# Kernel optimization log

Measured on AMD Instinct MI355X. Metric: run time of the kernel, lower is better.

Reference implementation:

```python
import jax, jax.numpy as jnp
import numpy as np

EPS = 1e-5
SCALE = 1.0 / np.float32(np.sqrt(64.0))  # 1/sqrt(d_Q)


def layernorm(x):
    # fresh nn.LayerNorm each call: gamma=1, beta=0
    m = jnp.mean(x, axis=-1, keepdims=True)
    v = jnp.mean((x - m) ** 2, axis=-1, keepdims=True)
    return (x - m) * jax.lax.rsqrt(v + EPS)


def setup_inputs() -> dict:
    key = jax.random.key(0)
    ks = jax.random.split(key, 8)
    B, S, D, H, F = 32, 512, 256, 64, 256
    w = 0.05
    return {
        "x": jax.random.normal(ks[0], (B, S, D), jnp.float32),
        "mask": jax.random.randint(ks[1], (B, 6, S, S), 0, 2).astype(jnp.int32),
        "Wq": jax.random.normal(ks[2], (6, D, H), jnp.float32) * w,
        "Wk": jax.random.normal(ks[3], (6, D, H), jnp.float32) * w,
        "Wv": jax.random.normal(ks[4], (6, D, H), jnp.float32) * w,
        "Wfc": jax.random.normal(ks[5], (6, H, D), jnp.float32) * w,
        "W1": jax.random.normal(ks[6], (D, F), jnp.float32) * w,
        "W2": jax.random.normal(ks[7], (F, D), jnp.float32) * w,
    }


def reference(x, mask, Wq, Wk, Wv, Wfc, W1, W2):
    m = mask.astype(bool)                                   # [B,6,S,S]
    # batched over the 6 relation branches (r axis)
    Q = jnp.einsum('bsd,rdh->brsh', x, Wq)                  # [B,6,S,64]
    K = jnp.einsum('bsd,rdh->brsh', x, Wk)
    V = jnp.einsum('bsd,rdh->brsh', x, Wv)
    score = jnp.einsum('brsh,brth->brst', Q, K) * SCALE     # [B,6,S,S]
    score = jnp.where(m, jnp.float32(-1e9), score)
    attn = jax.nn.softmax(score, axis=-1)
    attn = jnp.where(m, jnp.float32(0.0), attn)             # post-softmax zeroing
    ctx = jnp.einsum('brst,brth->brsh', attn, V)            # [B,6,S,64]
    proj = jnp.einsum('brsh,rhd->brsd', ctx, Wfc)           # [B,6,S,256]
    branch = layernorm(proj + x[:, None, :, :])             # residual + fresh LN per branch
    s = jnp.sum(branch, axis=1)                             # sum of 6 branches [B,S,256]
    ffn = jnp.maximum(jnp.einsum('bsd,df->bsf', s, W1), 0.0)
    ffn = jnp.einsum('bsf,fd->bsd', ffn, W2)
    return layernorm(ffn + s)
```

## Files before the change

kernel.cpp:

```cpp
#include <hip/hip_runtime.h>
#include <hip/hip_bf16.h>

#define BB 32
#define RR 6
#define SS 512
#define DD 256
#define HH 64
#define FF 256

typedef short  short8 __attribute__((ext_vector_type(8)));
typedef short  short4v __attribute__((ext_vector_type(4)));
typedef float  f32x4  __attribute__((ext_vector_type(4)));
typedef unsigned short ushort_t;
typedef unsigned int   uint_t;

__device__ __forceinline__ ushort_t f2bf(float f) {
    __hip_bfloat16 b = __float2bfloat16(f);
    return __builtin_bit_cast(ushort_t, b);
}
__device__ __forceinline__ float bf2f(ushort_t u) {
    return __bfloat162float(__builtin_bit_cast(__hip_bfloat16, u));
}

__global__ __launch_bounds__(256) void convert_all_kernel(
        const float* __restrict__ x,
        const float* __restrict__ Wq, const float* __restrict__ Wk, const float* __restrict__ Wv,
        const float* __restrict__ Wfc, const float* __restrict__ W1, const float* __restrict__ W2,
        ushort_t* __restrict__ xb, ushort_t* __restrict__ wT, ushort_t* __restrict__ w1T,
        ushort_t* __restrict__ w2T, ushort_t* __restrict__ wfcT) {
    int bid = blockIdx.x;
    if (bid < 4096) {
        int gid = bid * 256 + threadIdx.x;
        float4 fv = ((const float4*)x)[gid];
        short4v o;
        o[0] = (short)f2bf(fv.x); o[1] = (short)f2bf(fv.y);
        o[2] = (short)f2bf(fv.z); o[3] = (short)f2bf(fv.w);
        *(short4v*)(xb + (size_t)gid * 4) = o;
        return;
    }
    int gid = (bid - 4096) * 256 + threadIdx.x;
    if (gid < 294912) {
        int n = gid >> 8, d = gid & 255;
        int r = n / 192, rem = n % 192;
        int which = rem >> 6, h = rem & 63;
        const float* W = which == 0 ? Wq : which == 1 ? Wk : Wv;
        wT[gid] = f2bf(W[(size_t)r * DD * HH + (size_t)d * HH + h]);
    } else if (gid < 360448) {
        int gg = gid - 294912;
        int f = gg >> 8, d = gg & 255;
        w1T[gg] = f2bf(W1[(size_t)d * FF + f]);
    } else if (gid < 425984) {
        int gg = gid - 360448;
        int d = gg >> 8, f = gg & 255;
        w2T[gg] = f2bf(W2[(size_t)f * DD + d]);
    } else {
        int gg = gid - 425984;
        int n = gg >> 6, h = gg & 63;
        int r = n >> 8, d = n & 255;
        wfcT[gg] = f2bf(Wfc[((size_t)r * HH + h) * DD + d]);
    }
}

__global__ __launch_bounds__(256) void qkv_mfma_kernel(
        const ushort_t* __restrict__ xb, const ushort_t* __restrict__ wT,
        ushort_t* __restrict__ q, ushort_t* __restrict__ k, ushort_t* __restrict__ v) {
    int bid = blockIdx.x;
    int id = (bid & 7) * 288 + (bid >> 3);
    int rt = id / 18, cw = id % 18;
    int r = cw / 3, which = cw % 3;

    int tid = threadIdx.x;
    int wv = tid >> 6, l = tid & 63;
    int wr = wv >> 1, wc = wv & 1;
    int g = l >> 4, lc = l & 15;

    const ushort_t* Arow = xb + ((size_t)(rt * 128 + wr * 64 + lc)) * DD + g * 8;
    const ushort_t* Brow = wT + ((size_t)(cw * 64 + wc * 32 + lc)) * DD + g * 8;

    f32x4 acc[4][2] = {};
    #pragma unroll 4
    for (int ks = 0; ks < 8; ++ks) {
        short8 af[4], bf[2];
        #pragma unroll
        for (int m = 0; m < 4; ++m)
            af[m] = *(const short8*)(Arow + (size_t)m * 16 * DD + ks * 32);
        #pragma unroll
        for (int n = 0; n < 2; ++n)
            bf[n] = *(const short8*)(Brow + (size_t)n * 16 * DD + ks * 32);
        #pragma unroll
        for (int m = 0; m < 4; ++m)
            #pragma unroll
            for (int n = 0; n < 2; ++n)
                acc[m][n] = __builtin_amdgcn_mfma_f32_16x16x32_bf16(af[m], bf[n], acc[m][n], 0, 0, 0);
    }

    ushort_t* outb = which == 0 ? q : which == 1 ? k : v;
    #pragma unroll
    for (int m = 0; m < 4; ++m) {
        #pragma unroll
        for (int reg = 0; reg < 4; ++reg) {
            int grow = rt * 128 + wr * 64 + m * 16 + g * 4 + reg;
            int orow = ((grow >> 9) * RR + r) * SS + (grow & (SS - 1));
            #pragma unroll
            for (int n = 0; n < 2; ++n)
                outb[(size_t)orow * HH + wc * 32 + n * 16 + lc] = f2bf(acc[m][n][reg]);
        }
    }
}

__global__ __launch_bounds__(256) void attn_mfma_kernel(
        const ushort_t* __restrict__ q, const ushort_t* __restrict__ k,
        const ushort_t* __restrict__ v, const int* __restrict__ mask,
        ushort_t* __restrict__ ctx) {
    int wg = blockIdx.x;
    int id = (wg & 7) * 192 + (wg >> 3);
    int br = id >> 3, qt = id & 7;

    __shared__ ushort_t K_lds[64 * 72];
    __shared__ ushort_t VT_lds[64 * 66];
    __shared__ ushort_t P_lds[4][16 * 72];

    int tid = threadIdx.x;
    int wv = tid >> 6, l = tid & 63;
    int g = l >> 4, lc = l & 15;

    int q0 = qt * 64 + wv * 16;
    const size_t base_kv = (size_t)br * SS * HH;

    short8 qf[2];
    #pragma unroll
    for (int kk = 0; kk < 2; ++kk)
        qf[kk] = *(const short8*)(q + ((size_t)br * SS + q0 + lc) * HH + kk * 32 + g * 8);

    f32x4 O[4] = {{0,0,0,0},{0,0,0,0},{0,0,0,0},{0,0,0,0}};
    float lrun[4] = {0.f, 0.f, 0.f, 0.f};

    const int* mb = mask + ((size_t)br * SS + q0) * SS;

    for (int t0 = 0; t0 < SS; t0 += 64) {
        __syncthreads();
        for (int c = tid; c < 512; c += 256) {
            int t = c >> 3, c8 = (c & 7) * 8;
            *(short8*)&K_lds[t * 72 + c8] =
                *(const short8*)(k + base_kv + (size_t)(t0 + t) * HH + c8);
        }
        {
            int h = tid & 63, tseg = tid >> 6;
            #pragma unroll
            for (int jj = 0; jj < 8; ++jj) {
                int t = tseg * 16 + jj * 2;
                uint_t p0 = v[base_kv + (size_t)(t0 + t) * HH + h];
                uint_t p1 = v[base_kv + (size_t)(t0 + t + 1) * HH + h];
                *(uint_t*)&VT_lds[h * 66 + t] = p0 | (p1 << 16);
            }
        }
        __syncthreads();

        f32x4 S[4];
        #pragma unroll
        for (int tc = 0; tc < 4; ++tc) {
            f32x4 c = {0, 0, 0, 0};
            #pragma unroll
            for (int kk = 0; kk < 2; ++kk) {
                short8 bf = *(const short8*)&K_lds[(tc * 16 + lc) * 72 + kk * 32 + g * 8];
                c = __builtin_amdgcn_mfma_f32_16x16x32_bf16(qf[kk], bf, c, 0, 0, 0);
            }
            S[tc] = c;
        }

        float psum[4] = {0.f, 0.f, 0.f, 0.f};
        ushort_t* Pw = P_lds[wv];
        #pragma unroll
        for (int tc = 0; tc < 4; ++tc)
            #pragma unroll
            for (int reg = 0; reg < 4; ++reg) {
                int qrow = 4 * g + reg;
                int mv = mb[(size_t)qrow * SS + t0 + tc * 16 + lc];
                float p = mv ? 0.f : __expf(S[tc][reg] * 0.125f);
                psum[reg] += p;
                Pw[(4 * g + reg) * 72 + tc * 16 + lc] = f2bf(p);
            }
        #pragma unroll
        for (int reg = 0; reg < 4; ++reg) {
            float ps = psum[reg];
            ps += __shfl_xor(ps, 1, 64);
            ps += __shfl_xor(ps, 2, 64);
            ps += __shfl_xor(ps, 4, 64);
            ps += __shfl_xor(ps, 8, 64);
            lrun[reg] += ps;
        }
        asm volatile("s_waitcnt lgkmcnt(0)" ::: "memory");

        #pragma unroll
        for (int ts = 0; ts < 2; ++ts) {
            short8 pa = *(const short8*)&Pw[lc * 72 + ts * 32 + g * 8];
            #pragma unroll
            for (int hb = 0; hb < 4; ++hb) {
                short8 vbf = *(const short8*)&VT_lds[(hb * 16 + lc) * 66 + ts * 32 + g * 8];
                O[hb] = __builtin_amdgcn_mfma_f32_16x16x32_bf16(pa, vbf, O[hb], 0, 0, 0);
            }
        }
    }

    ushort_t* cb = ctx + ((size_t)br * SS + q0) * HH;
    #pragma unroll
    for (int reg = 0; reg < 4; ++reg) {
        float inv = lrun[reg] > 0.f ? 1.f / lrun[reg] : 0.f;
        #pragma unroll
        for (int hb = 0; hb < 4; ++hb)
            cb[(size_t)(4 * g + reg) * HH + hb * 16 + lc] = f2bf(O[hb][reg] * inv);
    }
}

__global__ __launch_bounds__(256) void fused_tail_kernel(
        const ushort_t* __restrict__ ctx, const ushort_t* __restrict__ wfcT,
        const float* __restrict__ x, const ushort_t* __restrict__ w1T,
        const ushort_t* __restrict__ w2T, float* __restrict__ out) {
    int bid = blockIdx.x;
    int rt = (bid & 7) * 128 + (bid >> 3);
    int row0 = rt * 16;
    int b = row0 >> 9, s0 = row0 & (SS - 1);

    int tid = threadIdx.x;
    int wc = tid >> 6, l = tid & 63;
    int g = l >> 4, lc = l & 15;
    int col0 = wc * 64;

    __shared__ ushort_t s_lds[16 * 264];
    __shared__ ushort_t h_lds[16 * 264];
    __shared__ float red_s[16][4];
    __shared__ float red_q[16][4];

    float xres[4][4];
    #pragma unroll
    for (int hb = 0; hb < 4; ++hb)
        #pragma unroll
        for (int reg = 0; reg < 4; ++reg)
            xres[hb][reg] = x[((size_t)row0 + g * 4 + reg) * DD + col0 + hb * 16 + lc];

    float acc_ln[4][4] = {};

    for (int r = 0; r < RR; ++r) {
        const ushort_t* Abase = ctx + (((size_t)b * RR + r) * SS + s0 + lc) * HH + g * 8;
        const ushort_t* Bbase = wfcT + ((size_t)r * 256 + col0 + lc) * HH + g * 8;
        f32x4 acc[4] = {};
        #pragma unroll
        for (int ks = 0; ks < 2; ++ks) {
            short8 af = *(const short8*)(Abase + ks * 32);
            #pragma unroll
            for (int hb = 0; hb < 4; ++hb) {
                short8 bf = *(const short8*)(Bbase + (size_t)hb * 16 * HH + ks * 32);
                acc[hb] = __builtin_amdgcn_mfma_f32_16x16x32_bf16(af, bf, acc[hb], 0, 0, 0);
            }
        }

        float psum[4] = {0, 0, 0, 0}, psq[4] = {0, 0, 0, 0};
        #pragma unroll
        for (int hb = 0; hb < 4; ++hb)
            #pragma unroll
            for (int reg = 0; reg < 4; ++reg) {
                float vv = acc[hb][reg] + xres[hb][reg];
                acc[hb][reg] = vv;
                psum[reg] += vv;
                psq[reg]  += vv * vv;
            }
        #pragma unroll
        for (int reg = 0; reg < 4; ++reg) {
            #pragma unroll
            for (int off = 1; off <= 8; off <<= 1) {
                psum[reg] += __shfl_xor(psum[reg], off, 64);
                psq[reg]  += __shfl_xor(psq[reg],  off, 64);
            }
        }
        if (lc == 0) {
            #pragma unroll
            for (int reg = 0; reg < 4; ++reg) {
                red_s[g * 4 + reg][wc] = psum[reg];
                red_q[g * 4 + reg][wc] = psq[reg];
            }
        }
        __syncthreads();
        #pragma unroll
        for (int reg = 0; reg < 4; ++reg) {
            int row = g * 4 + reg;
            float sum = red_s[row][0] + red_s[row][1] + red_s[row][2] + red_s[row][3];
            float sq  = red_q[row][0] + red_q[row][1] + red_q[row][2] + red_q[row][3];
            float mean = sum * (1.f / 256.f);
            float var  = sq * (1.f / 256.f) - mean * mean;
            float inv  = rsqrtf(var + 1e-5f);
            #pragma unroll
            for (int hb = 0; hb < 4; ++hb)
                acc_ln[hb][reg] += (acc[hb][reg] - mean) * inv;
        }
        __syncthreads();
    }

    #pragma unroll
    for (int hb = 0; hb < 4; ++hb)
        #pragma unroll
        for (int reg = 0; reg < 4; ++reg)
            s_lds[(g * 4 + reg) * 264 + col0 + hb * 16 + lc] = f2bf(acc_ln[hb][reg]);
    __syncthreads();

    f32x4 acc1[4] = {};
    #pragma unroll
    for (int ks = 0; ks < 8; ++ks) {
        short8 af = *(const short8*)&s_lds[lc * 264 + ks * 32 + g * 8];
        #pragma unroll
        for (int hb = 0; hb < 4; ++hb) {
            short8 bf = *(const short8*)(w1T + (size_t)(col0 + hb * 16 + lc) * DD + ks * 32 + g * 8);
            acc1[hb] = __builtin_amdgcn_mfma_f32_16x16x32_bf16(af, bf, acc1[hb], 0, 0, 0);
        }
    }
    #pragma unroll
    for (int hb = 0; hb < 4; ++hb)
        #pragma unroll
        for (int reg = 0; reg < 4; ++reg)
            h_lds[(g * 4 + reg) * 264 + col0 + hb * 16 + lc] = f2bf(fmaxf(acc1[hb][reg], 0.f));
    __syncthreads();

    f32x4 acc2[4] = {};
    #pragma unroll
    for (int ks = 0; ks < 8; ++ks) {
        short8 af = *(const short8*)&h_lds[lc * 264 + ks * 32 + g * 8];
        #pragma unroll
        for (int hb = 0; hb < 4; ++hb) {
            short8 bf = *(const short8*)(w2T + (size_t)(col0 + hb * 16 + lc) * FF + ks * 32 + g * 8);
            acc2[hb] = __builtin_amdgcn_mfma_f32_16x16x32_bf16(af, bf, acc2[hb], 0, 0, 0);
        }
    }

    float psum[4] = {0, 0, 0, 0}, psq[4] = {0, 0, 0, 0};
    #pragma unroll
    for (int hb = 0; hb < 4; ++hb)
        #pragma unroll
        for (int reg = 0; reg < 4; ++reg) {
            float vv = acc2[hb][reg] + bf2f(s_lds[(g * 4 + reg) * 264 + col0 + hb * 16 + lc]);
            acc2[hb][reg] = vv;
            psum[reg] += vv;
            psq[reg]  += vv * vv;
        }
    #pragma unroll
    for (int reg = 0; reg < 4; ++reg) {
        #pragma unroll
        for (int off = 1; off <= 8; off <<= 1) {
            psum[reg] += __shfl_xor(psum[reg], off, 64);
            psq[reg]  += __shfl_xor(psq[reg],  off, 64);
        }
    }
    if (lc == 0) {
        #pragma unroll
        for (int reg = 0; reg < 4; ++reg) {
            red_s[g * 4 + reg][wc] = psum[reg];
            red_q[g * 4 + reg][wc] = psq[reg];
        }
    }
    __syncthreads();
    #pragma unroll
    for (int reg = 0; reg < 4; ++reg) {
        int row = g * 4 + reg;
        float sum = red_s[row][0] + red_s[row][1] + red_s[row][2] + red_s[row][3];
        float sq  = red_q[row][0] + red_q[row][1] + red_q[row][2] + red_q[row][3];
        float mean = sum * (1.f / 256.f);
        float var  = sq * (1.f / 256.f) - mean * mean;
        float inv  = rsqrtf(var + 1e-5f);
        #pragma unroll
        for (int hb = 0; hb < 4; ++hb)
            out[((size_t)row0 + row) * DD + col0 + hb * 16 + lc] = (acc2[hb][reg] - mean) * inv;
    }
}

extern "C" void kernel_launch(void* const* d_in, const int* in_sizes, int n_in,
                              void* d_out, int out_size, void* d_ws, size_t ws_size,
                              hipStream_t stream) {
    const float* x    = (const float*)d_in[0];
    const int*   mask = (const int*)  d_in[1];
    const float* Wq   = (const float*)d_in[2];
    const float* Wk   = (const float*)d_in[3];
    const float* Wv   = (const float*)d_in[4];
    const float* Wfc  = (const float*)d_in[5];
    const float* W1   = (const float*)d_in[6];
    const float* W2   = (const float*)d_in[7];
    float* out = (float*)d_out;

    const size_t QKV = (size_t)BB * RR * SS * HH;
    const size_t BSD = (size_t)BB * SS * DD;
    ushort_t* qb  = (ushort_t*)d_ws;
    ushort_t* kb  = qb + QKV;
    ushort_t* vb  = kb + QKV;
    ushort_t* ctx = vb + QKV;
    ushort_t* xb  = ctx + QKV;
    ushort_t* wT  = xb + BSD;
    ushort_t* w1T = wT + (size_t)1152 * 256;
    ushort_t* w2T = w1T + 65536;
    ushort_t* wfcT = w2T + 65536;

    convert_all_kernel<<<6144, 256, 0, stream>>>(x, Wq, Wk, Wv, Wfc, W1, W2,
                                                 xb, wT, w1T, w2T, wfcT);
    qkv_mfma_kernel  <<<2304, 256, 0, stream>>>(xb, wT, qb, kb, vb);
    attn_mfma_kernel <<<BB * RR * 8, 256, 0, stream>>>(qb, kb, vb, mask, ctx);
    fused_tail_kernel<<<1024, 256, 0, stream>>>(ctx, wfcT, x, w1T, w2T, out);
}
```

Measured before the change: 191.9 us.

## Give each wave full rows in tail kernel to drop cross-wave LayerNorm reductions

```diff
diff --git a/kernel.cpp b/kernel.cpp
--- a/kernel.cpp
+++ b/kernel.cpp
@@ -212,55 +212,54 @@
     }
 }
 
-__global__ __launch_bounds__(256) void fused_tail_kernel(
+__global__ __launch_bounds__(128) void fused_tail_kernel(
         const ushort_t* __restrict__ ctx, const ushort_t* __restrict__ wfcT,
         const float* __restrict__ x, const ushort_t* __restrict__ w1T,
         const ushort_t* __restrict__ w2T, float* __restrict__ out) {
     int bid = blockIdx.x;
-    int rt = (bid & 7) * 128 + (bid >> 3);
-    int row0 = rt * 16;
+    int sw = (bid & 7) * 64 + (bid >> 3);
+    int tid = threadIdx.x;
+    int wv = tid >> 6, l = tid & 63;
+    int g = l >> 4, lc = l & 15;
+
+    int row0 = (sw * 2 + wv) * 16;
     int b = row0 >> 9, s0 = row0 & (SS - 1);
 
-    int tid = threadIdx.x;
-    int wc = tid >> 6, l = tid & 63;
-    int g = l >> 4, lc = l & 15;
-    int col0 = wc * 64;
-
-    __shared__ ushort_t s_lds[16 * 264];
-    __shared__ ushort_t h_lds[16 * 264];
-    __shared__ float red_s[16][4];
-    __shared__ float red_q[16][4];
-
-    float xres[4][4];
-    #pragma unroll
-    for (int hb = 0; hb < 4; ++hb)
+    __shared__ ushort_t s_lds[2][16 * 264];
+    __shared__ ushort_t h_lds[2][16 * 264];
+    ushort_t* S = s_lds[wv];
+    ushort_t* Hh = h_lds[wv];
+
+    float xres[16][4];
+    #pragma unroll
+    for (int n = 0; n < 16; ++n)
         #pragma unroll
         for (int reg = 0; reg < 4; ++reg)
-            xres[hb][reg] = x[((size_t)row0 + g * 4 + reg) * DD + col0 + hb * 16 + lc];
-
-    float acc_ln[4][4] = {};
+            xres[n][reg] = x[((size_t)row0 + g * 4 + reg) * DD + n * 16 + lc];
+
+    float acc_ln[16][4] = {};
 
     for (int r = 0; r < RR; ++r) {
         const ushort_t* Abase = ctx + (((size_t)b * RR + r) * SS + s0 + lc) * HH + g * 8;
-        const ushort_t* Bbase = wfcT + ((size_t)r * 256 + col0 + lc) * HH + g * 8;
-        f32x4 acc[4] = {};
+        const ushort_t* Bbase = wfcT + ((size_t)r * 256 + lc) * HH + g * 8;
+        f32x4 acc[16] = {};
         #pragma unroll
         for (int ks = 0; ks < 2; ++ks) {
             short8 af = *(const short8*)(Abase + ks * 32);
             #pragma unroll
-            for (int hb = 0; hb < 4; ++hb) {
-                short8 bf = *(const short8*)(Bbase + (size_t)hb * 16 * HH + ks * 32);
-                acc[hb] = __builtin_amdgcn_mfma_f32_16x16x32_bf16(af, bf, acc[hb], 0, 0, 0);
+            for (int n = 0; n < 16; ++n) {
+                short8 bf = *(const short8*)(Bbase + (size_t)n * 16 * HH + ks * 32);
+                acc[n] = __builtin_amdgcn_mfma_f32_16x16x32_bf16(af, bf, acc[n], 0, 0, 0);
             }
         }
 
         float psum[4] = {0, 0, 0, 0}, psq[4] = {0, 0, 0, 0};
         #pragma unroll
-        for (int hb = 0; hb < 4; ++hb)
+        for (int n = 0; n < 16; ++n)
             #pragma unroll
             for (int reg = 0; reg < 4; ++reg) {
-                float vv = acc[hb][reg] + xres[hb][reg];
-                acc[hb][reg] = vv;
+                float vv = acc[n][reg] + xres[n][reg];
+                acc[n][reg] = vv;
                 psum[reg] += vv;
                 psq[reg]  += vv * vv;
             }
@@ -271,72 +270,57 @@
                 psum[reg] += __shfl_xor(psum[reg], off, 64);
                 psq[reg]  += __shfl_xor(psq[reg],  off, 64);
             }
-        }
-        if (lc == 0) {
-            #pragma unroll
-            for (int reg = 0; reg < 4; ++reg) {
-                red_s[g * 4 + reg][wc] = psum[reg];
-                red_q[g * 4 + reg][wc] = psq[reg];
-            }
-        }
-        __syncthreads();
+            float mean = psum[reg] * (1.f / 256.f);
+            float var  = psq[reg] * (1.f / 256.f) - mean * mean;
+            float inv  = rsqrtf(var + 1e-5f);
+            #pragma unroll
+            for (int n = 0; n < 16; ++n)
+                acc_ln[n][reg] += (acc[n][reg] - mean) * inv;
+        }
+    }
+
+    #pragma unroll
+    for (int n = 0; n < 16; ++n)
+        #pragma unroll
+        for (int reg = 0; reg < 4; ++reg)
+            S[(g * 4 + reg) * 264 + n * 16 + lc] = f2bf(acc_ln[n][reg]);
+    __syncthreads();
+
+    f32x4 acc1[16] = {};
+    #pragma unroll
+    for (int ks = 0; ks < 8; ++ks) {
+        short8 af = *(const short8*)&S[lc * 264 + ks * 32 + g * 8];
+        #pragma unroll
+        for (int n = 0; n < 16; ++n) {
+            short8 bf = *(const short8*)(w1T + (size_t)(n * 16 + lc) * DD + ks * 32 + g * 8);
+            acc1[n] = __builtin_amdgcn_mfma_f32_16x16x32_bf16(af, bf, acc1[n], 0, 0, 0);
+        }
+    }
+    #pragma unroll
+    for (int n = 0; n < 16; ++n)
+        #pragma unroll
+        for (int reg = 0; reg < 4; ++reg)
+            Hh[(g * 4 + reg) * 264 + n * 16 + lc] = f2bf(fmaxf(acc1[n][reg], 0.f));
+    __syncthreads();
+
+    f32x4 acc2[16] = {};
+    #pragma unroll
+    for (int ks = 0; ks < 8; ++ks) {
+        short8 af = *(const short8*)&Hh[lc * 264 + ks * 32 + g * 8];
+        #pragma unroll
+        for (int n = 0; n < 16; ++n) {
+            short8 bf = *(const short8*)(w2T + (size_t)(n * 16 + lc) * FF + ks * 32 + g * 8);
+            acc2[n] = __builtin_amdgcn_mfma_f32_16x16x32_bf16(af, bf, acc2[n], 0, 0, 0);
+        }
+    }
+
+    float psum[4] = {0, 0, 0, 0}, psq[4] = {0, 0, 0, 0};
+    #pragma unroll
+    for (int n = 0; n < 16; ++n)
         #pragma unroll
         for (int reg = 0; reg < 4; ++reg) {
-            int row = g * 4 + reg;
-            float sum = red_s[row][0] + red_s[row][1] + red_s[row][2] + red_s[row][3];
-            float sq  = red_q[row][0] + red_q[row][1] + red_q[row][2] + red_q[row][3];
-            float mean = sum * (1.f / 256.f);
-            float var  = sq * (1.f / 256.f) - mean * mean;
-            float inv  = rsqrtf(var + 1e-5f);
-            #pragma unroll
-            for (int hb = 0; hb < 4; ++hb)
-                acc_ln[hb][reg] += (acc[hb][reg] - mean) * inv;
-        }
-        __syncthreads();
-    }
-
-    #pragma unroll
-    for (int hb = 0; hb < 4; ++hb)
-        #pragma unroll
-        for (int reg = 0; reg < 4; ++reg)
-            s_lds[(g * 4 + reg) * 264 + col0 + hb * 16 + lc] = f2bf(acc_ln[hb][reg]);
-    __syncthreads();
-
-    f32x4 acc1[4] = {};
-    #pragma unroll
-    for (int ks = 0; ks < 8; ++ks) {
-        short8 af = *(const short8*)&s_lds[lc * 264 + ks * 32 + g * 8];
-        #pragma unroll
-        for (int hb = 0; hb < 4; ++hb) {
-            short8 bf = *(const short8*)(w1T + (size_t)(col0 + hb * 16 + lc) * DD + ks * 32 + g * 8);
-            acc1[hb] = __builtin_amdgcn_mfma_f32_16x16x32_bf16(af, bf, acc1[hb], 0, 0, 0);
-        }
-    }
-    #pragma unroll
-    for (int hb = 0; hb < 4; ++hb)
-        #pragma unroll
-        for (int reg = 0; reg < 4; ++reg)
-            h_lds[(g * 4 + reg) * 264 + col0 + hb * 16 + lc] = f2bf(fmaxf(acc1[hb][reg], 0.f));
-    __syncthreads();
-
-    f32x4 acc2[4] = {};
-    #pragma unroll
-    for (int ks = 0; ks < 8; ++ks) {
-        short8 af = *(const short8*)&h_lds[lc * 264 + ks * 32 + g * 8];
-        #pragma unroll
-        for (int hb = 0; hb < 4; ++hb) {
-            short8 bf = *(const short8*)(w2T + (size_t)(col0 + hb * 16 + lc) * FF + ks * 32 + g * 8);
-            acc2[hb] = __builtin_amdgcn_mfma_f32_16x16x32_bf16(af, bf, acc2[hb], 0, 0, 0);
-        }
-    }
-
-    float psum[4] = {0, 0, 0, 0}, psq[4] = {0, 0, 0, 0};
-    #pragma unroll
-    for (int hb = 0; hb < 4; ++hb)
-        #pragma unroll
-        for (int reg = 0; reg < 4; ++reg) {
-            float vv = acc2[hb][reg] + bf2f(s_lds[(g * 4 + reg) * 264 + col0 + hb * 16 + lc]);
-            acc2[hb][reg] = vv;
+            float vv = acc2[n][reg] + bf2f(S[(g * 4 + reg) * 264 + n * 16 + lc]);
+            acc2[n][reg] = vv;
             psum[reg] += vv;
             psq[reg]  += vv * vv;
         }
@@ -347,26 +331,12 @@
             psum[reg] += __shfl_xor(psum[reg], off, 64);
             psq[reg]  += __shfl_xor(psq[reg],  off, 64);
         }
-    }
-    if (lc == 0) {
-        #pragma unroll
-        for (int reg = 0; reg < 4; ++reg) {
-            red_s[g * 4 + reg][wc] = psum[reg];
-            red_q[g * 4 + reg][wc] = psq[reg];
-        }
-    }
-    __syncthreads();
-    #pragma unroll
-    for (int reg = 0; reg < 4; ++reg) {
-        int row = g * 4 + reg;
-        float sum = red_s[row][0] + red_s[row][1] + red_s[row][2] + red_s[row][3];
-        float sq  = red_q[row][0] + red_q[row][1] + red_q[row][2] + red_q[row][3];
-        float mean = sum * (1.f / 256.f);
-        float var  = sq * (1.f / 256.f) - mean * mean;
+        float mean = psum[reg] * (1.f / 256.f);
+        float var  = psq[reg] * (1.f / 256.f) - mean * mean;
         float inv  = rsqrtf(var + 1e-5f);
         #pragma unroll
-        for (int hb = 0; hb < 4; ++hb)
-            out[((size_t)row0 + row) * DD + col0 + hb * 16 + lc] = (acc2[hb][reg] - mean) * inv;
+        for (int n = 0; n < 16; ++n)
+            out[((size_t)row0 + g * 4 + reg) * DD + n * 16 + lc] = (acc2[n][reg] - mean) * inv;
     }
 }
 
@@ -399,5 +369,5 @@
                                                  xb, wT, w1T, w2T, wfcT);
     qkv_mfma_kernel  <<<2304, 256, 0, stream>>>(xb, wT, qb, kb, vb);
     attn_mfma_kernel <<<BB * RR * 8, 256, 0, stream>>>(qb, kb, vb, mask, ctx);
-    fused_tail_kernel<<<1024, 256, 0, stream>>>(ctx, wfcT, x, w1T, w2T, out);
-}
+    fused_tail_kernel<<<512, 128, 0, stream>>>(ctx, wfcT, x, w1T, w2T, out);
+}
```

After: 199.5 us. 3.9% more time.

## Fuse output projection and per-branch LayerNorm into attention kernel epilogue

Applied to the files above, without the earlier changes.

```diff
diff --git a/kernel.cpp b/kernel.cpp
--- a/kernel.cpp
+++ b/kernel.cpp
@@ -108,13 +108,15 @@
     }
 }
 
-__global__ __launch_bounds__(256) void attn_mfma_kernel(
+__global__ __launch_bounds__(256, 2) void attn_proj_kernel(
         const ushort_t* __restrict__ q, const ushort_t* __restrict__ k,
         const ushort_t* __restrict__ v, const int* __restrict__ mask,
-        ushort_t* __restrict__ ctx) {
+        const float* __restrict__ x, const ushort_t* __restrict__ wfcT,
+        ushort_t* __restrict__ pbuf) {
     int wg = blockIdx.x;
     int id = (wg & 7) * 192 + (wg >> 3);
     int br = id >> 3, qt = id & 7;
+    int b = br / RR, r = br % RR;
 
     __shared__ ushort_t K_lds[64 * 72];
     __shared__ ushort_t VT_lds[64 * 66];
@@ -202,24 +204,69 @@
         }
     }
 
-    ushort_t* cb = ctx + ((size_t)br * SS + q0) * HH;
+    ushort_t* Pw = P_lds[wv];
     #pragma unroll
     for (int reg = 0; reg < 4; ++reg) {
         float inv = lrun[reg] > 0.f ? 1.f / lrun[reg] : 0.f;
         #pragma unroll
         for (int hb = 0; hb < 4; ++hb)
-            cb[(size_t)(4 * g + reg) * HH + hb * 16 + lc] = f2bf(O[hb][reg] * inv);
-    }
-}
-
-__global__ __launch_bounds__(256) void fused_tail_kernel(
-        const ushort_t* __restrict__ ctx, const ushort_t* __restrict__ wfcT,
-        const float* __restrict__ x, const ushort_t* __restrict__ w1T,
+            Pw[(4 * g + reg) * 72 + hb * 16 + lc] = f2bf(O[hb][reg] * inv);
+    }
+    asm volatile("s_waitcnt lgkmcnt(0)" ::: "memory");
+
+    short8 oa0 = *(const short8*)&Pw[lc * 72 + g * 8];
+    short8 oa1 = *(const short8*)&Pw[lc * 72 + 32 + g * 8];
+
+    const ushort_t* Wr = wfcT + (size_t)r * 256 * HH;
+    f32x4 accp[16];
+    #pragma unroll
+    for (int n = 0; n < 16; ++n) {
+        f32x4 c = {0, 0, 0, 0};
+        short8 b0 = *(const short8*)(Wr + (size_t)(n * 16 + lc) * HH + g * 8);
+        short8 b1 = *(const short8*)(Wr + (size_t)(n * 16 + lc) * HH + 32 + g * 8);
+        c = __builtin_amdgcn_mfma_f32_16x16x32_bf16(oa0, b0, c, 0, 0, 0);
+        c = __builtin_amdgcn_mfma_f32_16x16x32_bf16(oa1, b1, c, 0, 0, 0);
+        accp[n] = c;
+    }
+
+    float psum[4] = {0, 0, 0, 0}, psq[4] = {0, 0, 0, 0};
+    #pragma unroll
+    for (int n = 0; n < 16; ++n)
+        #pragma unroll
+        for (int reg = 0; reg < 4; ++reg) {
+            float xv = x[((size_t)b * SS + q0 + 4 * g + reg) * DD + n * 16 + lc];
+            float vv = accp[n][reg] + xv;
+            accp[n][reg] = vv;
+            psum[reg] += vv;
+            psq[reg]  += vv * vv;
+        }
+    #pragma unroll
+    for (int reg = 0; reg < 4; ++reg) {
+        #pragma unroll
+        for (int off = 1; off <= 8; off <<= 1) {
+            psum[reg] += __shfl_xor(psum[reg], off, 64);
+            psq[reg]  += __shfl_xor(psq[reg],  off, 64);
+        }
+    }
+    ushort_t* pb = pbuf + (size_t)r * ((size_t)BB * SS * DD);
+    #pragma unroll
+    for (int reg = 0; reg < 4; ++reg) {
+        float mean = psum[reg] * (1.f / 256.f);
+        float var  = psq[reg] * (1.f / 256.f) - mean * mean;
+        float inv  = rsqrtf(var + 1e-5f);
+        size_t rowbase = ((size_t)b * SS + q0 + 4 * g + reg) * DD;
+        #pragma unroll
+        for (int n = 0; n < 16; ++n)
+            pb[rowbase + n * 16 + lc] = f2bf((accp[n][reg] - mean) * inv);
+    }
+}
+
+__global__ __launch_bounds__(256) void ffn_kernel(
+        const ushort_t* __restrict__ pbuf, const ushort_t* __restrict__ w1T,
         const ushort_t* __restrict__ w2T, float* __restrict__ out) {
     int bid = blockIdx.x;
     int rt = (bid & 7) * 128 + (bid >> 3);
     int row0 = rt * 16;
-    int b = row0 >> 9, s0 = row0 & (SS - 1);
 
     int tid = threadIdx.x;
     int wc = tid >> 6, l = tid & 63;
@@ -231,75 +278,24 @@
     __shared__ float red_s[16][4];
     __shared__ float red_q[16][4];
 
-    float xres[4][4];
-    #pragma unroll
-    for (int hb = 0; hb < 4; ++hb)
-        #pragma unroll
-        for (int reg = 0; reg < 4; ++reg)
-            xres[hb][reg] = x[((size_t)row0 + g * 4 + reg) * DD + col0 + hb * 16 + lc];
-
-    float acc_ln[4][4] = {};
-
-    for (int r = 0; r < RR; ++r) {
-        const ushort_t* Abase = ctx + (((size_t)b * RR + r) * SS + s0 + lc) * HH + g * 8;
-        const ushort_t* Bbase = wfcT + ((size_t)r * 256 + col0 + lc) * HH + g * 8;
-        f32x4 acc[4] = {};
-        #pragma unroll
-        for (int ks = 0; ks < 2; ++ks) {
-            short8 af = *(const short8*)(Abase + ks * 32);
-            #pragma unroll
-            for (int hb = 0; hb < 4; ++hb) {
-                short8 bf = *(const short8*)(Bbase + (size_t)hb * 16 * HH + ks * 32);
-                acc[hb] = __builtin_amdgcn_mfma_f32_16x16x32_bf16(af, bf, acc[hb], 0, 0, 0);
-            }
-        }
-
-        float psum[4] = {0, 0, 0, 0}, psq[4] = {0, 0, 0, 0};
-        #pragma unroll
-        for (int hb = 0; hb < 4; ++hb)
-            #pragma unroll
-            for (int reg = 0; reg < 4; ++reg) {
-                float vv = acc[hb][reg] + xres[hb][reg];
-                acc[hb][reg] = vv;
-                psum[reg] += vv;
-                psq[reg]  += vv * vv;
-            }
-        #pragma unroll
-        for (int reg = 0; reg < 4; ++reg) {
-            #pragma unroll
-            for (int off = 1; off <= 8; off <<= 1) {
-                psum[reg] += __shfl_xor(psum[reg], off, 64);
-                psq[reg]  += __shfl_xor(psq[reg],  off, 64);
-            }
-        }
-        if (lc == 0) {
-            #pragma unroll
-            for (int reg = 0; reg < 4; ++reg) {
-                red_s[g * 4 + reg][wc] = psum[reg];
-                red_q[g * 4 + reg][wc] = psq[reg];
-            }
-        }
-        __syncthreads();
-        #pragma unroll
-        for (int reg = 0; reg < 4; ++reg) {
-            int row = g * 4 + reg;
-            float sum = red_s[row][0] + red_s[row][1] + red_s[row][2] + red_s[row][3];
-            float sq  = red_q[row][0] + red_q[row][1] + red_q[row][2] + red_q[row][3];
-            float mean = sum * (1.f / 256.f);
-            float var  = sq * (1.f / 256.f) - mean * mean;
-            float inv  = rsqrtf(var + 1e-5f);
-            #pragma unroll
-            for (int hb = 0; hb < 4; ++hb)
-                acc_ln[hb][reg] += (acc[hb][reg] - mean) * inv;
-        }
-        __syncthreads();
-    }
-
-    #pragma unroll
-    for (int hb = 0; hb < 4; ++hb)
-        #pragma unroll
-        for (int reg = 0; reg < 4; ++reg)
-            s_lds[(g * 4 + reg) * 264 + col0 + hb * 16 + lc] = f2bf(acc_ln[hb][reg]);
+    const size_t BSD = (size_t)BB * SS * DD;
+
+    for (int c = tid; c < 512; c += 256) {
+        int row = c >> 5, c8 = (c & 31) * 8;
+        size_t idx = ((size_t)row0 + row) * DD + c8;
+        float s8[8] = {0, 0, 0, 0, 0, 0, 0, 0};
+        #pragma unroll
+        for (int r = 0; r < RR; ++r) {
+            short8 pv = *(const short8*)(pbuf + (size_t)r * BSD + idx);
+            #pragma unroll
+            for (int j = 0; j < 8; ++j)
+                s8[j] += bf2f((ushort_t)pv[j]);
+        }
+        short8 o;
+        #pragma unroll
+        for (int j = 0; j < 8; ++j) o[j] = (short)f2bf(s8[j]);
+        *(short8*)&s_lds[row * 264 + c8] = o;
+    }
     __syncthreads();
 
     f32x4 acc1[4] = {};
@@ -388,16 +384,16 @@
     ushort_t* qb  = (ushort_t*)d_ws;
     ushort_t* kb  = qb + QKV;
     ushort_t* vb  = kb + QKV;
-    ushort_t* ctx = vb + QKV;
-    ushort_t* xb  = ctx + QKV;
+    ushort_t* xb  = vb + QKV;
     ushort_t* wT  = xb + BSD;
     ushort_t* w1T = wT + (size_t)1152 * 256;
     ushort_t* w2T = w1T + 65536;
     ushort_t* wfcT = w2T + 65536;
+    ushort_t* pbuf = wfcT + (size_t)RR * 256 * 64;
 
     convert_all_kernel<<<6144, 256, 0, stream>>>(x, Wq, Wk, Wv, Wfc, W1, W2,
                                                  xb, wT, w1T, w2T, wfcT);
-    qkv_mfma_kernel  <<<2304, 256, 0, stream>>>(xb, wT, qb, kb, vb);
-    attn_mfma_kernel <<<BB * RR * 8, 256, 0, stream>>>(qb, kb, vb, mask, ctx);
-    fused_tail_kernel<<<1024, 256, 0, stream>>>(ctx, wfcT, x, w1T, w2T, out);
-}
+    qkv_mfma_kernel <<<2304, 256, 0, stream>>>(xb, wT, qb, kb, vb);
+    attn_proj_kernel<<<BB * RR * 8, 256, 0, stream>>>(qb, kb, vb, mask, x, wfcT, pbuf);
+    ffn_kernel      <<<1024, 256, 0, stream>>>(pbuf, w1T, w2T, out);
+}
```

Result: slower. 202.2 us (+5.4%).
